# Kernel tuning notes

Measured on AMD Instinct MI355X. Metric: run time of the kernel, lower is better.

The kernel has to match this reference:

```python
import jax, jax.numpy as jnp
import numpy as np
import math

B, C, SEG, SEGLEN, K, GROUPS, WG = 8, 256, 40, 200, 10, 32, 4
L4 = SEGLEN // 4            # 50 temporal slots per segment
N = SEG * L4                # 2000 total points
WIDTH = GROUPS * WG         # 128 bottleneck width


def build_neighbor_idx(seg_lens):
    """Exact numpy replication of torch get_temporal_graph's neighbor-list loop.
    Returns flat (into B*N rows) neighbor indices of shape (B, N, 3)."""
    seg_lens = np.asarray(seg_lens)
    Bn, S = seg_lens.shape
    nb = np.zeros((Bn, S * L4, 3), dtype=np.int64)
    for i in range(Bn):
        last_valid = 0
        skip_seg = 0
        base = i * S * L4
        for j in range(S):
            valid = math.ceil(seg_lens[i, j] / 4.0)
            for k in range(L4):
                idx = j * L4 + k
                if k < valid:
                    nb[i, idx] = [base + last_valid, base + idx, base + idx]
                    last_valid = idx
                    if k == 0 and j != 0:
                        nb[i, skip_seg, 2] = base + idx
                    if k == valid - 1:
                        skip_seg = idx
                    else:
                        nb[i, idx, 2] = base + idx + 1
                else:
                    nb[i, idx] = [base + idx] * 3
    return nb


def conv1x1(x, W, b):
    # x: (B, Cin, N, T), W: (Cout, Cin)
    return jnp.einsum('bcnt,oc->bont', x, W) + b[None, :, None, None]


def grouped_1x3(x, W, b):
    # x: (B, WIDTH, N, 3), W: (WIDTH, WIDTH//GROUPS, 3); valid conv -> T_out = 1
    Bn, _, Nn, _ = x.shape
    xg = x.reshape(Bn, GROUPS, WIDTH // GROUPS, Nn, 3)
    Wg = W.reshape(GROUPS, WIDTH // GROUPS, WIDTH // GROUPS, 3)
    y = jnp.einsum('bgcnt,goct->bgon', xg, Wg)
    return y.reshape(Bn, WIDTH, Nn, 1) + b[None, :, None, None]


def grouped_1x1(x, W, b):
    # x: (B, WIDTH, N, T), W: (WIDTH, WIDTH//GROUPS)
    Bn, _, Nn, T = x.shape
    xg = x.reshape(Bn, GROUPS, WIDTH // GROUPS, Nn, T)
    Wg = W.reshape(GROUPS, WIDTH // GROUPS, WIDTH // GROUPS)
    y = jnp.einsum('bgcnt,goc->bgont', xg, Wg)
    return y.reshape(Bn, WIDTH, Nn, T) + b[None, :, None, None]


def setup_inputs() -> dict:
    key = jax.random.key(0)
    ks = jax.random.split(key, 10)
    s = 0.05
    x = jax.random.normal(ks[0], (B, C, N), dtype=jnp.float32)
    seg_lens = jax.random.randint(ks[1], (B, SEG), 0, 201)
    neighbor_idx = jnp.asarray(build_neighbor_idx(np.asarray(seg_lens)))
    return dict(
        x=x, seg_lens=seg_lens, neighbor_idx=neighbor_idx,
        tW1=jax.random.normal(ks[2], (WIDTH, C), jnp.float32) * s,
        tb1=jnp.zeros((WIDTH,), jnp.float32),
        tW2=jax.random.normal(ks[3], (WIDTH, WIDTH // GROUPS, 3), jnp.float32) * s,
        tb2=jnp.zeros((WIDTH,), jnp.float32),
        tW3=jax.random.normal(ks[4], (C, WIDTH), jnp.float32) * s,
        tb3=jnp.zeros((C,), jnp.float32),
        sW1=jax.random.normal(ks[5], (WIDTH, 2 * C), jnp.float32) * s,
        sb1=jnp.zeros((WIDTH,), jnp.float32),
        sW2=jax.random.normal(ks[6], (WIDTH, WIDTH // GROUPS), jnp.float32) * s,
        sb2=jnp.zeros((WIDTH,), jnp.float32),
        sW3=jax.random.normal(ks[7], (C, WIDTH), jnp.float32) * s,
        sb3=jnp.zeros((C,), jnp.float32),
    )


def reference(x, seg_lens, neighbor_idx, tW1, tb1, tW2, tb2, tW3, tb3,
              sW1, sb1, sW2, sb2, sW3, sb3):
    relu = jax.nn.relu
    B_, C_, N_ = x.shape
    flat = x.transpose(0, 2, 1).reshape(B_ * N_, C_)  # (B*N, C)

    # --- temporal branch: gather 3 temporal-graph neighbors -> (B, C, N, 3) ---
    tg = flat[neighbor_idx.reshape(-1)].reshape(B_, N_, 3, C_).transpose(0, 3, 1, 2)
    h = relu(conv1x1(tg, tW1, tb1))
    h = relu(grouped_1x3(h, tW2, tb2))
    tout = conv1x1(h, tW3, tb3).max(axis=-1)  # (B, C, N)

    # --- semantic branch: kNN graph feature (style=1) ---
    xx = jnp.sum(x * x, axis=1)                       # (B, N)
    inner = jnp.einsum('bci,bcj->bij', x, x)          # (B, N, N)
    pd = 2.0 * inner - xx[:, None, :] - xx[:, :, None]  # negative sq. distances
    _, idx = jax.lax.top_k(pd, K)                     # (B, N, K)
    base = (jnp.arange(B_) * N_)[:, None, None]
    nbr = flat[(idx + base).reshape(-1)].reshape(B_, N_, K, C_)
    center = jnp.broadcast_to(x.transpose(0, 2, 1)[:, :, None, :], (B_, N_, K, C_))
    xf = jnp.concatenate([nbr, center], axis=3).transpose(0, 3, 1, 2)  # (B, 2C, N, K)
    g = relu(conv1x1(xf, sW1, sb1))
    g = relu(grouped_1x1(g, sW2, sb2))
    sout = conv1x1(g, sW3, sb3).max(axis=-1)  # (B, C, N)

    return relu(tout + x + sout)
```

## Files before the change

kernel.cpp:

```cpp
#include <hip/hip_runtime.h>

#define NPTS 2000
#define NBATCH 8
#define NC 256
#define NW 128
#define NK 10
#define NROWS (NBATCH * NPTS)
#define JPAD 2048
#define PL2 (JPAD * 32)

typedef _Float16 f16x8 __attribute__((ext_vector_type(8)));
typedef _Float16 f16x4 __attribute__((ext_vector_type(4)));
typedef float f32x4 __attribute__((ext_vector_type(4)));

__device__ __forceinline__ float dot4(float4 a, float4 b) {
    return a.x*b.x + a.y*b.y + a.z*b.z + a.w*b.w;
}
__device__ __forceinline__ float4 relu4(float4 a) {
    return make_float4(fmaxf(a.x,0.f), fmaxf(a.y,0.f), fmaxf(a.z,0.f), fmaxf(a.w,0.f));
}
__device__ __forceinline__ float4 add4(float4 a, float4 b) {
    return make_float4(a.x+b.x, a.y+b.y, a.z+b.z, a.w+b.w);
}

__device__ __forceinline__ void ins10(float d, int j, float* vals, int* idxs) {
    if (d > vals[9]) {
        float v = d; int id = j;
        #pragma unroll
        for (int s = 0; s < 10; ++s) {
            if (v > vals[s]) {
                float tv = vals[s]; vals[s] = v; v = tv;
                int   ti = idxs[s]; idxs[s] = id; id = ti;
            }
        }
    }
}

__device__ __forceinline__ void gl_lds16(const void* g, void* l) {
    __builtin_amdgcn_global_load_lds(
        (const __attribute__((address_space(1))) void*)g,
        (__attribute__((address_space(3))) void*)l, 16, 0, 0);
}

__global__ __launch_bounds__(256) void k_prep(
    const float* __restrict__ x, _Float16* __restrict__ xb,
    float* __restrict__ xx)
{
    __shared__ float T[64][259];
    __shared__ float Pp[64][4];
    const int t  = threadIdx.x;
    const int b  = blockIdx.x >> 5;
    const int n0 = (blockIdx.x & 31) * 64;

    #pragma unroll
    for (int p = 0; p < 64; ++p) {
        const int idx = p*256 + t;
        const int c = idx >> 6, nl = idx & 63;
        T[nl][c] = x[((size_t)b*NC + c)*NPTS + min(n0 + nl, NPTS-1)];
    }
    __syncthreads();

    const int row = t & 63, q = t >> 6;
    const int gr  = n0 + row;
    const bool ok = gr < NPTS;
    const int sw  = (gr >> 1) & 3;
    float ss = 0.f;
    #pragma unroll
    for (int u = 0; u < 2; ++u) {
        const int kc = 2*q + u;
        const size_t bh = ((size_t)(b*8 + kc)*2    )*PL2 + (size_t)gr*32;
        const size_t bl = ((size_t)(b*8 + kc)*2 + 1)*PL2 + (size_t)gr*32;
        #pragma unroll
        for (int g = 0; g < 4; ++g) {
            f16x8 vh, vl;
            #pragma unroll
            for (int e = 0; e < 8; ++e) {
                const float f = ok ? T[row][kc*32 + g*8 + e] : 0.f;
                ss = fmaf(f, f, ss);
                const _Float16 h = (_Float16)f;
                vh[e] = h;
                vl[e] = (_Float16)(f - (float)h);
            }
            *(f16x8*)&xb[bh + (g ^ sw)*8] = vh;
            *(f16x8*)&xb[bl + (g ^ sw)*8] = vl;
        }
    }
    Pp[row][q] = ss;
    __syncthreads();
    if (t < 64 && n0 + t < NPTS)
        xx[(size_t)b*NPTS + n0 + t] = Pp[t][0] + Pp[t][1] + Pp[t][2] + Pp[t][3];
}

__global__ __launch_bounds__(256) void k_wprep(const float* __restrict__ a,
                                               _Float16* __restrict__ o, int n)
{
    const int i = (blockIdx.x*256 + threadIdx.x)*4;
    if (i < n) {
        const float4 v = *(const float4*)&a[i];
        f16x4 h = {(_Float16)v.x, (_Float16)v.y, (_Float16)v.z, (_Float16)v.w};
        *(f16x4*)&o[i] = h;
    }
}

__global__ __launch_bounds__(256) void k_rowgemm(
    const float* __restrict__ x,
    const float* __restrict__ tW1, const float* __restrict__ tb1,
    const float* __restrict__ sW1, const float* __restrict__ sb1,
    float* __restrict__ T1r, float* __restrict__ P, float* __restrict__ Q)
{
    __shared__ float Xs[32][34];
    __shared__ float Ws[32][132];
    const int t  = threadIdx.x;
    const int r0 = blockIdx.x * 32;
    const int sel = blockIdx.y;
    const int jq = t & 15,  iq = t >> 4;
    const int j0 = jq * 8,  i0 = iq * 2;

    float acc[2][8];
    #pragma unroll
    for (int a = 0; a < 2; ++a)
        #pragma unroll
        for (int q = 0; q < 8; ++q) acc[a][q] = 0.f;

    const int li = t & 31;
    const int lk = t >> 5;
    const int rl = r0 + li;
    const int lb = rl / NPTS, ln = rl % NPTS;

    for (int c0 = 0; c0 < NC; c0 += 32) {
        #pragma unroll
        for (int p = 0; p < 4; ++p) {
            int kk = lk + p * 8;
            Xs[kk][li] = x[((size_t)lb * NC + c0 + kk) * NPTS + ln];
        }
        #pragma unroll
        for (int jj = 0; jj < 16; ++jj) {
            int j = jj * 8 + lk;
            int c = c0 + li;
            float w;
            if (sel == 0)      w = tW1[j * NC + c];
            else if (sel == 1) w = sW1[j * (2*NC) + c];
            else               w = sW1[j * (2*NC) + NC + c];
            Ws[li][j] = w;
        }
        __syncthreads();
        #pragma unroll 8
        for (int kk = 0; kk < 32; ++kk) {
            const float2 xv = *(const float2*)&Xs[kk][i0];
            const float4 w0 = *(const float4*)&Ws[kk][j0];
            const float4 w1 = *(const float4*)&Ws[kk][j0 + 4];
            float w[8] = {w0.x,w0.y,w0.z,w0.w,w1.x,w1.y,w1.z,w1.w};
            #pragma unroll
            for (int q = 0; q < 8; ++q) {
                acc[0][q] = fmaf(xv.x, w[q], acc[0][q]);
                acc[1][q] = fmaf(xv.y, w[q], acc[1][q]);
            }
        }
        __syncthreads();
    }

    #pragma unroll
    for (int a = 0; a < 2; ++a) {
        const int r = r0 + i0 + a;
        float o[8];
        #pragma unroll
        for (int q = 0; q < 8; ++q) {
            float v = acc[a][q];
            if (sel == 0)      { v += tb1[j0+q]; v = fmaxf(v, 0.f); }
            else if (sel == 2) { v += sb1[j0+q]; }
            o[q] = v;
        }
        float* dst = (sel==0 ? T1r : (sel==1 ? P : Q)) + (size_t)r * NW + j0;
        *(float4*)dst       = make_float4(o[0],o[1],o[2],o[3]);
        *(float4*)(dst + 4) = make_float4(o[4],o[5],o[6],o[7]);
    }
}

__global__ __launch_bounds__(256, 3) void k_topk(
    const _Float16* __restrict__ xb, const float* __restrict__ xx,
    float* __restrict__ pval, int* __restrict__ pidx)
{
    __shared__ __align__(16) char smem[32768];

    const int t    = threadIdx.x;
    const int b    = blockIdx.x & 7;
    const int ig   = (blockIdx.x >> 3) & 31;
    const int jh   = blockIdx.x >> 8;
    const int i0   = ig * 64;
    const int lane = t & 63;
    const int w    = t >> 6;
    const int lr   = lane & 15, rg = lane >> 4;
    const size_t bbase = (size_t)b * 16 * PL2;

    f16x8 bh[8], bl[8];
    {
        const int i = min(i0 + w*16 + lr, NPTS - 1);
        const int sw = (i >> 1) & 3;
        const int go = (rg ^ sw) * 8;
        #pragma unroll
        for (int kc = 0; kc < 8; ++kc) {
            const size_t ph = bbase + (size_t)(kc*2)*PL2 + (size_t)i*32 + go;
            bh[kc] = *(const f16x8*)&xb[ph];
            bl[kc] = *(const f16x8*)&xb[ph + PL2];
        }
    }

    float vals[10]; int idxs[10];
    #pragma unroll
    for (int s = 0; s < 10; ++s) { vals[s] = -3.0e38f; idxs[s] = 0x7fffffff; }

    const float* xxp = xx + (size_t)b * NPTS;
    const char*  gb  = (const char*)xb + bbase*2;

    const int jt0 = (jh == 0) ? 0 : (jh == 1 ? 42 : 84);
    const int jt1 = (jh == 0) ? 42 : (jh == 1 ? 84 : 125);

    #pragma unroll
    for (int q = 0; q < 4; ++q) {
        const int p = w*4 + q;
        gl_lds16(gb + (size_t)p*(PL2*2) + (size_t)jt0*1024 + lane*16,
                 smem + ((jt0 & 1)*16384) + p*1024);
    }

    const int ao = lr*64 + ((rg ^ ((lr >> 1) & 3)) << 4);

    for (int jt = jt0; jt < jt1; ++jt) {
        __syncthreads();

        if (jt + 1 < jt1) {
            char* ld = smem + (((jt+1) & 1)*16384);
            #pragma unroll
            for (int q = 0; q < 4; ++q) {
                const int p = w*4 + q;
                gl_lds16(gb + (size_t)p*(PL2*2) + (size_t)(jt+1)*1024 + lane*16,
                         ld + p*1024);
            }
        }

        f32x4 acc = {0.f,0.f,0.f,0.f};
        {
            const char* Bb = smem + (jt & 1)*16384;
            #pragma unroll
            for (int kc = 0; kc < 8; ++kc) {
                const f16x8 ah = *(const f16x8*)(Bb + (kc*2    )*1024 + ao);
                const f16x8 al = *(const f16x8*)(Bb + (kc*2 + 1)*1024 + ao);
                acc = __builtin_amdgcn_mfma_f32_16x16x32_f16(ah, bh[kc], acc, 0,0,0);
                acc = __builtin_amdgcn_mfma_f32_16x16x32_f16(ah, bl[kc], acc, 0,0,0);
                acc = __builtin_amdgcn_mfma_f32_16x16x32_f16(al, bh[kc], acc, 0,0,0);
            }
        }

        {
            const int j0r = jt*16 + rg*4;
            const f32x4 xv = *(const f32x4*)&xxp[j0r];
            const float d0 = 2.f*acc[0] - xv[0];
            const float d1 = 2.f*acc[1] - xv[1];
            const float d2 = 2.f*acc[2] - xv[2];
            const float d3 = 2.f*acc[3] - xv[3];
            const float mx = fmaxf(fmaxf(d0, d1), fmaxf(d2, d3));
            if (mx > vals[9]) {
                ins10(d0, j0r,     vals, idxs);
                ins10(d1, j0r + 1, vals, idxs);
                ins10(d2, j0r + 2, vals, idxs);
                ins10(d3, j0r + 3, vals, idxs);
            }
        }
    }

    __syncthreads();
    float* mval = (float*)smem;
    int*   midx = (int*)(smem + 10240);
    {
        const int g = w*16 + lr;
        #pragma unroll
        for (int s = 0; s < 10; ++s) {
            mval[(g*4 + rg)*10 + s] = vals[s];
            midx[(g*4 + rg)*10 + s] = idxs[s];
        }
    }
    __syncthreads();
    if (t < 128) {
        const int g = t >> 1, pr = t & 1;
        float* va = &mval[(g*4 + pr)*10];     int* ia = &midx[(g*4 + pr)*10];
        const float* vb = &mval[(g*4 + pr + 2)*10]; const int* ib = &midx[(g*4 + pr + 2)*10];
        float ov[10]; int oi[10]; int pa = 0, pb = 0;
        #pragma unroll
        for (int s = 0; s < 10; ++s) {
            const float A = va[pa], Bv = vb[pb];
            const int  Ai = ia[pa], Bi = ib[pb];
            const bool ta = (A > Bv) || (A == Bv && Ai < Bi);
            ov[s] = ta ? A : Bv; oi[s] = ta ? Ai : Bi;
            pa += ta ? 1 : 0; pb += ta ? 0 : 1;
        }
        #pragma unroll
        for (int s = 0; s < 10; ++s) { va[s] = ov[s]; ia[s] = oi[s]; }
    }
    __syncthreads();
    if (t < 64) {
        const int g = t;
        const int i = i0 + g;
        if (i < NPTS) {
            const float* va = &mval[(g*4 + 0)*10]; const int* ia = &midx[(g*4 + 0)*10];
            const float* vb = &mval[(g*4 + 1)*10]; const int* ib = &midx[(g*4 + 1)*10];
            float* ov = &pval[((size_t)(b*NPTS + i)*3 + jh)*10];
            int*   oi = &pidx[((size_t)(b*NPTS + i)*3 + jh)*10];
            int pa = 0, pb = 0;
            #pragma unroll
            for (int s = 0; s < 10; ++s) {
                const float A = va[pa], Bv = vb[pb];
                const int  Ai = ia[pa], Bi = ib[pb];
                const bool ta = (A > Bv) || (A == Bv && Ai < Bi);
                ov[s] = ta ? A : Bv; oi[s] = ta ? Ai : Bi;
                pa += ta ? 1 : 0; pb += ta ? 0 : 1;
            }
        }
    }
}

__global__ __launch_bounds__(256) void k_tkmerge(
    const float* __restrict__ pval, const int* __restrict__ pidx,
    int* __restrict__ tk)
{
    const int r = blockIdx.x*256 + threadIdx.x;
    if (r >= NROWS) return;
    const float* v  = &pval[(size_t)r*30];
    const int*   ix = &pidx[(size_t)r*30];
    const int base = (r / NPTS) * NPTS;
    int* op = &tk[(size_t)r*NK];
    int p0 = 0, p1 = 0, p2 = 0;
    #pragma unroll
    for (int s = 0; s < NK; ++s) {
        float bv = -3.4e38f; int bi = 0x7fffffff; int bl = 0;
        {
            const float vv = v[p0];       const int ii = ix[p0];
            if (vv > bv || (vv == bv && ii < bi)) { bv = vv; bi = ii; bl = 0; }
        }
        {
            const float vv = v[10 + p1];  const int ii = ix[10 + p1];
            if (vv > bv || (vv == bv && ii < bi)) { bv = vv; bi = ii; bl = 1; }
        }
        {
            const float vv = v[20 + p2];  const int ii = ix[20 + p2];
            if (vv > bv || (vv == bv && ii < bi)) { bv = vv; bi = ii; bl = 2; }
        }
        p0 += (bl == 0); p1 += (bl == 1); p2 += (bl == 2);
        op[s] = base + bi;
    }
}

#define AST 136
__global__ __launch_bounds__(256, 2) void k_fused(
    const float* __restrict__ x,
    const int* __restrict__ nb, const int* __restrict__ tk,
    const float* __restrict__ T1r, const float* __restrict__ P, const float* __restrict__ Q,
    const float* __restrict__ tW2, const float* __restrict__ tb2,
    const float* __restrict__ sW2, const float* __restrict__ sb2,
    const _Float16* __restrict__ wt3h, const _Float16* __restrict__ ws3h,
    const float* __restrict__ tb3, const float* __restrict__ sb3,
    float* __restrict__ out)
{
    __shared__ __align__(16) _Float16 A16[144*AST];
    __shared__ float Ssm[8][260];
    __shared__ float Zr[8][260];

    const int t  = threadIdx.x;
    const int r0 = blockIdx.x * 8;
    const int bb = r0 / NPTS;
    const int n0 = r0 % NPTS;

    {
        const float4 z4 = make_float4(0.f,0.f,0.f,0.f);
        float4* p4 = (float4*)A16;
        #pragma unroll
        for (int i = 0; i < 10; ++i) {
            const int idx = t + i*256;
            if (idx < 2448) p4[idx] = z4;
        }
    }
    __syncthreads();

    {
        const int o    = t & 127;
        const int half = t >> 7;
        const int g4   = o & ~3;

        const float4 f0 = *(const float4*)&tW2[o*12];
        const float4 f1 = *(const float4*)&tW2[o*12 + 4];
        const float4 f2 = *(const float4*)&tW2[o*12 + 8];
        const float4 wt0 = make_float4(f0.x, f0.w, f1.z, f2.y);
        const float4 wt1 = make_float4(f0.y, f1.x, f1.w, f2.z);
        const float4 wt2 = make_float4(f0.z, f1.y, f2.x, f2.w);
        const float4 wsw = *(const float4*)&sW2[o*4];
        const float tb2o = tb2[o], sb2o = sb2[o];

        #pragma unroll
        for (int ptl = 0; ptl < 4; ++ptl) {
            const int pt = half*4 + ptl;
            const int r  = r0 + pt;
            const int nb0 = nb[r*3+0], nb1 = nb[r*3+1], nb2 = nb[r*3+2];
            int ki[NK];
            #pragma unroll
            for (int k = 0; k < NK; ++k) ki[k] = tk[r*NK + k];
            const float4 h0 = *(const float4*)&T1r[(size_t)nb0*NW + g4];
            const float4 h1 = *(const float4*)&T1r[(size_t)nb1*NW + g4];
            const float4 h2 = *(const float4*)&T1r[(size_t)nb2*NW + g4];
            const float4 qf = *(const float4*)&Q[(size_t)r*NW + g4];
            float4 pf[NK];
            #pragma unroll
            for (int k = 0; k < NK; ++k) pf[k] = *(const float4*)&P[(size_t)ki[k]*NW + g4];

            const float z = tb2o + dot4(wt0,h0) + dot4(wt1,h1) + dot4(wt2,h2);
            A16[(128 + pt)*AST + o] = (_Float16)fmaxf(z, 0.f);
            #pragma unroll
            for (int k = 0; k < NK; ++k) {
                const float4 g1 = relu4(add4(pf[k], qf));
                A16[(pt*16 + k)*AST + o] = (_Float16)fmaxf(dot4(wsw, g1) + sb2o, 0.f);
            }
        }
    }
    __syncthreads();

    const int lane = t & 63, w = t >> 6;
    const int lr = lane & 15, lg = lane >> 4;
    const int n0w = w * 64;

    f32x4 accG[8][4] = {};
    f32x4 accZ[4] = {};

    #pragma unroll
    for (int kt = 0; kt < 4; ++kt) {
        const int ko = kt*32 + lg*8;
        f16x8 bs[4], bt[4];
        #pragma unroll
        for (int nt = 0; nt < 4; ++nt) {
            const int n = n0w + nt*16 + lr;
            bs[nt] = *(const f16x8*)&ws3h[n*NW + ko];
            bt[nt] = *(const f16x8*)&wt3h[n*NW + ko];
        }
        #pragma unroll
        for (int mt = 0; mt < 8; ++mt) {
            const f16x8 a = *(const f16x8*)&A16[(mt*16 + lr)*AST + ko];
            #pragma unroll
            for (int nt = 0; nt < 4; ++nt)
                accG[mt][nt] = __builtin_amdgcn_mfma_f32_16x16x32_f16(a, bs[nt], accG[mt][nt], 0,0,0);
        }
        const f16x8 az = *(const f16x8*)&A16[(128 + lr)*AST + ko];
        #pragma unroll
        for (int nt = 0; nt < 4; ++nt)
            accZ[nt] = __builtin_amdgcn_mfma_f32_16x16x32_f16(az, bt[nt], accZ[nt], 0,0,0);
    }

    const int rg = lg;
    #pragma unroll
    for (int mt = 0; mt < 8; ++mt) {
        #pragma unroll
        for (int nt = 0; nt < 4; ++nt) {
            float v;
            if (rg < 2)       v = fmaxf(fmaxf(accG[mt][nt][0], accG[mt][nt][1]),
                                        fmaxf(accG[mt][nt][2], accG[mt][nt][3]));
            else if (rg == 2) v = fmaxf(accG[mt][nt][0], accG[mt][nt][1]);
            else              v = -3.0e38f;
            v = fmaxf(v, __shfl_xor(v, 16));
            v = fmaxf(v, __shfl_xor(v, 32));
            if (lane < 16) Ssm[mt][n0w + nt*16 + lane] = v;
        }
    }
    #pragma unroll
    for (int nt = 0; nt < 4; ++nt) {
        #pragma unroll
        for (int q = 0; q < 4; ++q) {
            if (rg < 2) Zr[rg*4 + q][n0w + nt*16 + lr] = accZ[nt][q];
        }
    }
    __syncthreads();

    {
        const int c = t;
        const float tb = tb3[c], sb = sb3[c];
        const size_t go = ((size_t)bb*NC + c)*NPTS + n0;
        const float4 xv0 = *(const float4*)&x[go];
        const float4 xv1 = *(const float4*)&x[go + 4];
        const float xr[8] = {xv0.x,xv0.y,xv0.z,xv0.w, xv1.x,xv1.y,xv1.z,xv1.w};
        float ov[8];
        #pragma unroll
        for (int p = 0; p < 8; ++p)
            ov[p] = fmaxf(Zr[p][c] + tb + Ssm[p][c] + sb + xr[p], 0.f);
        *(float4*)&out[go]     = make_float4(ov[0],ov[1],ov[2],ov[3]);
        *(float4*)&out[go + 4] = make_float4(ov[4],ov[5],ov[6],ov[7]);
    }
}

extern "C" void kernel_launch(void* const* d_in, const int* in_sizes, int n_in,
                              void* d_out, int out_size, void* d_ws, size_t ws_size,
                              hipStream_t stream) {
    (void)in_sizes; (void)n_in; (void)out_size; (void)ws_size;
    const float* x   = (const float*)d_in[0];
    const int*   nb  = (const int*)d_in[2];
    const float* tW1 = (const float*)d_in[3];
    const float* tb1 = (const float*)d_in[4];
    const float* tW2 = (const float*)d_in[5];
    const float* tb2 = (const float*)d_in[6];
    const float* tW3 = (const float*)d_in[7];
    const float* tb3 = (const float*)d_in[8];
    const float* sW1 = (const float*)d_in[9];
    const float* sb1 = (const float*)d_in[10];
    const float* sW2 = (const float*)d_in[11];
    const float* sb2 = (const float*)d_in[12];
    const float* sW3 = (const float*)d_in[13];
    const float* sb3 = (const float*)d_in[14];
    float* out = (float*)d_out;

    float* ws  = (float*)d_ws;
    float* T1r  = ws;
    float* P    = ws + 2048000;
    float* Q    = ws + 4096000;
    float* xxp  = ws + 6144000;
    int*   tk   = (int*)(ws + 6160000);
    float* pval = ws + 6320000;
    int*   pidx = (int*)(ws + 6800000);
    _Float16* xb   = (_Float16*)(ws + 7280000);
    _Float16* wt3h = xb + (size_t)NBATCH * 16 * PL2;
    _Float16* ws3h = wt3h + NC * NW;

    k_prep<<<NBATCH * 32, 256, 0, stream>>>(x, xb, xxp);
    k_wprep<<<32, 256, 0, stream>>>(tW3, wt3h, NC * NW);
    k_wprep<<<32, 256, 0, stream>>>(sW3, ws3h, NC * NW);
    k_rowgemm<<<dim3(NROWS / 32, 3), 256, 0, stream>>>(x, tW1, tb1, sW1, sb1, T1r, P, Q);
    k_topk<<<768, 256, 0, stream>>>(xb, xxp, pval, pidx);
    k_tkmerge<<<(NROWS + 255) / 256, 256, 0, stream>>>(pval, pidx, tk);
    k_fused<<<NROWS / 8, 256, 0, stream>>>(x, nb, tk, T1r, P, Q,
                                           tW2, tb2, sW2, sb2, wt3h, ws3h, tb3, sb3, out);
}
```

Before: 448.4 us.

## Load kNN candidate tiles directly from global instead of LDS double-buffering

The top-k distance kernel stops staging candidate-point fp16 tiles into LDS with async global-to-LDS loads and double buffering. Each wave now reads its A fragments straight from global memory, relying on L2/L1 since all four waves read the same tiles. The squared norms for the block's candidate range are cached once in LDS. The XOR swizzle in the prep kernel's layout is removed to match. This drops the per-tile barriers and the LDS traffic, but every wave now issues redundant global loads with no explicit prefetch, so load latency may be exposed.

```diff
diff --git a/kernel.cpp b/kernel.cpp
--- a/kernel.cpp
+++ b/kernel.cpp
@@ -34,12 +34,6 @@
             }
         }
     }
-}
-
-__device__ __forceinline__ void gl_lds16(const void* g, void* l) {
-    __builtin_amdgcn_global_load_lds(
-        (const __attribute__((address_space(1))) void*)g,
-        (__attribute__((address_space(3))) void*)l, 16, 0, 0);
 }
 
 __global__ __launch_bounds__(256) void k_prep(
@@ -63,7 +57,6 @@
     const int row = t & 63, q = t >> 6;
     const int gr  = n0 + row;
     const bool ok = gr < NPTS;
-    const int sw  = (gr >> 1) & 3;
     float ss = 0.f;
     #pragma unroll
     for (int u = 0; u < 2; ++u) {
@@ -81,8 +74,8 @@
                 vh[e] = h;
                 vl[e] = (_Float16)(f - (float)h);
             }
-            *(f16x8*)&xb[bh + (g ^ sw)*8] = vh;
-            *(f16x8*)&xb[bl + (g ^ sw)*8] = vl;
+            *(f16x8*)&xb[bh + g*8] = vh;
+            *(f16x8*)&xb[bl + g*8] = vl;
         }
     }
     Pp[row][q] = ss;
@@ -180,7 +173,8 @@
     const _Float16* __restrict__ xb, const float* __restrict__ xx,
     float* __restrict__ pval, int* __restrict__ pidx)
 {
-    __shared__ __align__(16) char smem[32768];
+    __shared__ __align__(16) char smem[20480];
+    float* xxs = (float*)smem;
 
     const int t    = threadIdx.x;
     const int b    = blockIdx.x & 7;
@@ -191,15 +185,21 @@
     const int w    = t >> 6;
     const int lr   = lane & 15, rg = lane >> 4;
     const size_t bbase = (size_t)b * 16 * PL2;
+    const int jbase  = jh * 672;
+    const int ntiles = (jh == 2) ? 41 : 42;
+
+    {
+        const int ncnt = ntiles * 16;
+        for (int idx = t; idx < ncnt; idx += 256)
+            xxs[idx] = xx[(size_t)b*NPTS + jbase + idx];
+    }
 
     f16x8 bh[8], bl[8];
     {
         const int i = min(i0 + w*16 + lr, NPTS - 1);
-        const int sw = (i >> 1) & 3;
-        const int go = (rg ^ sw) * 8;
         #pragma unroll
         for (int kc = 0; kc < 8; ++kc) {
-            const size_t ph = bbase + (size_t)(kc*2)*PL2 + (size_t)i*32 + go;
+            const size_t ph = bbase + (size_t)(kc*2)*PL2 + (size_t)i*32 + rg*8;
             bh[kc] = *(const f16x8*)&xb[ph];
             bl[kc] = *(const f16x8*)&xb[ph + PL2];
         }
@@ -209,60 +209,45 @@
     #pragma unroll
     for (int s = 0; s < 10; ++s) { vals[s] = -3.0e38f; idxs[s] = 0x7fffffff; }
 
-    const float* xxp = xx + (size_t)b * NPTS;
-    const char*  gb  = (const char*)xb + bbase*2;
-
-    const int jt0 = (jh == 0) ? 0 : (jh == 1 ? 42 : 84);
-    const int jt1 = (jh == 0) ? 42 : (jh == 1 ? 84 : 125);
-
-    #pragma unroll
-    for (int q = 0; q < 4; ++q) {
-        const int p = w*4 + q;
-        gl_lds16(gb + (size_t)p*(PL2*2) + (size_t)jt0*1024 + lane*16,
-                 smem + ((jt0 & 1)*16384) + p*1024);
-    }
-
-    const int ao = lr*64 + ((rg ^ ((lr >> 1) & 3)) << 4);
-
-    for (int jt = jt0; jt < jt1; ++jt) {
-        __syncthreads();
-
-        if (jt + 1 < jt1) {
-            char* ld = smem + (((jt+1) & 1)*16384);
-            #pragma unroll
-            for (int q = 0; q < 4; ++q) {
-                const int p = w*4 + q;
-                gl_lds16(gb + (size_t)p*(PL2*2) + (size_t)(jt+1)*1024 + lane*16,
-                         ld + p*1024);
-            }
-        }
+    __syncthreads();
+
+    for (int jt = 0; jt < ntiles; ++jt) {
+        const int j0 = jbase + jt*16;
+        const size_t ja = (size_t)(j0 + lr)*32 + rg*8;
 
         f32x4 acc = {0.f,0.f,0.f,0.f};
+        #pragma unroll
+        for (int h = 0; h < 2; ++h) {
+            f16x8 ah[4], al[4];
+            #pragma unroll
+            for (int k4 = 0; k4 < 4; ++k4) {
+                const int kc = h*4 + k4;
+                ah[k4] = *(const f16x8*)&xb[bbase + (size_t)(kc*2    )*PL2 + ja];
+                al[k4] = *(const f16x8*)&xb[bbase + (size_t)(kc*2 + 1)*PL2 + ja];
+            }
+            #pragma unroll
+            for (int k4 = 0; k4 < 4; ++k4) {
+                const int kc = h*4 + k4;
+                acc = __builtin_amdgcn_mfma_f32_16x16x32_f16(ah[k4], bh[kc], acc, 0,0,0);
+                acc = __builtin_amdgcn_mfma_f32_16x16x32_f16(ah[k4], bl[kc], acc, 0,0,0);
+                acc = __builtin_amdgcn_mfma_f32_16x16x32_f16(al[k4], bh[kc], acc, 0,0,0);
+            }
+        }
+
         {
-            const char* Bb = smem + (jt & 1)*16384;
-            #pragma unroll
-            for (int kc = 0; kc < 8; ++kc) {
-                const f16x8 ah = *(const f16x8*)(Bb + (kc*2    )*1024 + ao);
-                const f16x8 al = *(const f16x8*)(Bb + (kc*2 + 1)*1024 + ao);
-                acc = __builtin_amdgcn_mfma_f32_16x16x32_f16(ah, bh[kc], acc, 0,0,0);
-                acc = __builtin_amdgcn_mfma_f32_16x16x32_f16(ah, bl[kc], acc, 0,0,0);
-                acc = __builtin_amdgcn_mfma_f32_16x16x32_f16(al, bh[kc], acc, 0,0,0);
-            }
-        }
-
-        {
-            const int j0r = jt*16 + rg*4;
-            const f32x4 xv = *(const f32x4*)&xxp[j0r];
+            const int jr = jt*16 + rg*4;
+            const f32x4 xv = *(const f32x4*)&xxs[jr];
             const float d0 = 2.f*acc[0] - xv[0];
             const float d1 = 2.f*acc[1] - xv[1];
             const float d2 = 2.f*acc[2] - xv[2];
             const float d3 = 2.f*acc[3] - xv[3];
             const float mx = fmaxf(fmaxf(d0, d1), fmaxf(d2, d3));
             if (mx > vals[9]) {
-                ins10(d0, j0r,     vals, idxs);
-                ins10(d1, j0r + 1, vals, idxs);
-                ins10(d2, j0r + 2, vals, idxs);
-                ins10(d3, j0r + 3, vals, idxs);
+                const int jg = j0 + rg*4;
+                ins10(d0, jg,     vals, idxs);
+                ins10(d1, jg + 1, vals, idxs);
+                ins10(d2, jg + 2, vals, idxs);
+                ins10(d3, jg + 3, vals, idxs);
             }
         }
     }
```

Result: slower. 458.5 us (+2.3%).
